# Kernel optimization log

Measured on AMD Instinct MI355X. Metric: run time of the kernel, lower is better.

The kernel has to match this reference:

```python
import jax, jax.numpy as jnp
import numpy as np

D_MODEL = 1024
N_HEADS = 16
D_K = D_MODEL // N_HEADS


def setup_inputs() -> dict:
    key = jax.random.key(0)
    k1, k2, k3, k4, k5 = jax.random.split(key, 5)
    B, S = 2, 2048
    scale = 1.0 / np.sqrt(D_MODEL)
    return {
        "query": jax.random.normal(k1, (B, S, D_MODEL), dtype=jnp.float32),
        "mask": jnp.ones((B, S, S), dtype=jnp.int32),
        "W_qkv": jax.random.normal(k2, (D_MODEL, 3 * D_MODEL), dtype=jnp.float32) * scale,
        "b_qkv": jax.random.normal(k3, (3 * D_MODEL,), dtype=jnp.float32) * 0.02,
        "W_out": jax.random.normal(k4, (D_MODEL, D_MODEL), dtype=jnp.float32) * scale,
        "b_out": jax.random.normal(k5, (D_MODEL,), dtype=jnp.float32) * 0.02,
    }


def reference(query, mask, W_qkv, b_qkv, W_out, b_out):
    B, S, _ = query.shape
    # fused QKV projection (all from query, matching the torch module)
    qkv = query @ W_qkv + b_qkv                      # [B, S, 3*D]
    q, k, v = jnp.split(qkv, 3, axis=-1)
    # [B, H, S, d_k]
    q = q.reshape(B, S, N_HEADS, D_K).transpose(0, 2, 1, 3)
    k = k.reshape(B, S, N_HEADS, D_K).transpose(0, 2, 1, 3)
    v = v.reshape(B, S, N_HEADS, D_K).transpose(0, 2, 1, 3)
    # scaled dot-product attention with explicit scores
    scores = jnp.einsum("bhqd,bhkd->bhqk", q, k) / jnp.sqrt(jnp.float32(D_K))
    m = mask[:, None, :, :]                           # [B, 1, S, S] broadcast over heads
    scores = jnp.where(m == 0, jnp.float32(-1e9), scores)
    attn = jax.nn.softmax(scores, axis=-1)           # dropout p=0 in eval -> identity
    ctx = jnp.einsum("bhqk,bhkd->bhqd", attn, v)     # [B, H, S, d_k]
    ctx = ctx.transpose(0, 2, 1, 3).reshape(B, S, D_MODEL)
    return ctx @ W_out + b_out
```

## Files before the change

kernel.cpp:

```cpp
#include <hip/hip_runtime.h>
#include <stdint.h>
#include <stddef.h>

#define S_LEN 2048
#define NB    2
#define DM    1024
#define NH    16
#define DKH   64
#define NTOK  4096
#define QKV_N 3072
#define QSCALE 0.18033688f

typedef __attribute__((ext_vector_type(4))) float floatx4;
using half2v = __attribute__((ext_vector_type(2))) _Float16;
using half4v = __attribute__((ext_vector_type(4))) _Float16;
using half8v = __attribute__((ext_vector_type(8))) _Float16;
using fp16x2 = __attribute__((ext_vector_type(2))) __fp16;

#if __has_builtin(__builtin_amdgcn_exp2f)
#define EXP2F __builtin_amdgcn_exp2f
#else
#define EXP2F exp2f
#endif

__device__ __forceinline__ void glds16(const void* g, void* l) {
    __builtin_amdgcn_global_load_lds((const __attribute__((address_space(1))) void*)g,
                                     (__attribute__((address_space(3))) void*)l,
                                     16, 0, 0);
}

__global__ __launch_bounds__(256) void cast_f16_kernel(const float* __restrict__ in,
                                                       _Float16* __restrict__ out, int n4) {
    int i = blockIdx.x * blockDim.x + threadIdx.x;
    if (i < n4) {
        float4 v = ((const float4*)in)[i];
        half4v o = {(_Float16)v.x, (_Float16)v.y, (_Float16)v.z, (_Float16)v.w};
        ((half4v*)out)[i] = o;
    }
}

__global__ __launch_bounds__(1024) void transpose_cast_kernel(const float* __restrict__ in,
                                                              _Float16* __restrict__ out,
                                                              int R, int C) {
    __shared__ float t[32][33];
    int c0 = blockIdx.x * 32, r0 = blockIdx.y * 32;
    int x = threadIdx.x, y = threadIdx.y;
    t[y][x] = in[(size_t)(r0 + y) * C + c0 + x];
    __syncthreads();
    out[(size_t)(c0 + y) * R + r0 + x] = (_Float16)t[x][y];
}

__global__ __launch_bounds__(256) void mask_reduce_kernel(const int* __restrict__ mask,
                                                          int* __restrict__ f, int n4) {
    int i = blockIdx.x * blockDim.x + threadIdx.x;
    if (i < n4) {
        int4 v = ((const int4*)mask)[i];
        if (v.x == 0 || v.y == 0 || v.z == 0 || v.w == 0) *f = 0;
    }
}

template <int FINAL, int BN>
__global__ __launch_bounds__(256) void gemm_bt_kernel(const _Float16* __restrict__ A,
                                                      const _Float16* __restrict__ Bt,
                                                      const float* __restrict__ bias,
                                                      float* __restrict__ Cf,
                                                      _Float16* __restrict__ Ch,
                                                      _Float16* __restrict__ Vt,
                                                      int M, int N, int K) {
    constexpr int NJ = BN / 32;
    __shared__ _Float16 As[128 * 64];
    __shared__ _Float16 Bs[BN * 64];

    const int nt = blockIdx.x, mt = blockIdx.y;
    const int tid = threadIdx.x, wave = tid >> 6, lane = tid & 63;
    const int quad = lane >> 4, l16 = lane & 15;
    const int wm = wave >> 1, wn = wave & 1;

    floatx4 acc[4][NJ];
    #pragma unroll
    for (int i = 0; i < 4; ++i)
        #pragma unroll
        for (int j = 0; j < NJ; ++j)
            #pragma unroll
            for (int r = 0; r < 4; ++r) acc[i][j][r] = 0.0f;

    const _Float16* Ab = A + (size_t)mt * 128 * K;
    const _Float16* Bb = Bt + (size_t)nt * BN * K;

    for (int kt = 0; kt < K; kt += 64) {
        #pragma unroll
        for (int p = 0; p < 4; ++p) {
            int slot = p * 256 + wave * 64 + lane;
            int row = slot >> 3, cc = slot & 7, c = cc ^ (row & 7);
            glds16(Ab + (size_t)row * K + kt + c * 8, As + (size_t)(p * 256 + wave * 64) * 8);
        }
        #pragma unroll
        for (int p = 0; p < BN / 32; ++p) {
            int slot = p * 256 + wave * 64 + lane;
            int row = slot >> 3, cc = slot & 7, c = cc ^ (row & 7);
            glds16(Bb + (size_t)row * K + kt + c * 8, Bs + (size_t)(p * 256 + wave * 64) * 8);
        }
        __syncthreads();

        #pragma unroll
        for (int kk = 0; kk < 2; ++kk) {
            half8v af[4], bfr[NJ];
            #pragma unroll
            for (int i = 0; i < 4; ++i) {
                int row = wm * 64 + i * 16 + l16;
                int c = (kk * 4 + quad) ^ (row & 7);
                af[i] = *(const half8v*)(As + row * 64 + c * 8);
            }
            #pragma unroll
            for (int j = 0; j < NJ; ++j) {
                int row = wn * (BN / 2) + j * 16 + l16;
                int c = (kk * 4 + quad) ^ (row & 7);
                bfr[j] = *(const half8v*)(Bs + row * 64 + c * 8);
            }
            #pragma unroll
            for (int i = 0; i < 4; ++i)
                #pragma unroll
                for (int j = 0; j < NJ; ++j)
                    acc[i][j] = __builtin_amdgcn_mfma_f32_16x16x32_f16(af[i], bfr[j], acc[i][j], 0, 0, 0);
        }
        __syncthreads();
    }

    #pragma unroll
    for (int j = 0; j < NJ; ++j) {
        int n = nt * BN + wn * (BN / 2) + j * 16 + l16;
        float bv = bias[n];
        #pragma unroll
        for (int i = 0; i < 4; ++i) {
            int m0 = mt * 128 + wm * 64 + i * 16 + quad * 4;
            float v[4];
            #pragma unroll
            for (int r = 0; r < 4; ++r) v[r] = acc[i][j][r] + bv;
            if (FINAL) {
                #pragma unroll
                for (int r = 0; r < 4; ++r) Cf[(size_t)(m0 + r) * N + n] = v[r];
            } else {
                if (n < DM) {
                    #pragma unroll
                    for (int r = 0; r < 4; ++r) v[r] *= QSCALE;
                }
                if (n < 2 * DM) {
                    #pragma unroll
                    for (int r = 0; r < 4; ++r)
                        Ch[(size_t)(m0 + r) * QKV_N + n] = (_Float16)v[r];
                } else {
                    int bb = m0 >> 11, s = m0 & (S_LEN - 1);
                    half4v t = {(_Float16)v[0], (_Float16)v[1], (_Float16)v[2], (_Float16)v[3]};
                    *(half4v*)(Vt + ((size_t)bb * (NH * DKH) + (n - 2 * DM)) * S_LEN + s) = t;
                }
            }
        }
    }
}

__global__ __launch_bounds__(128) void flash_kernel(const _Float16* __restrict__ qkv,
                                                    const _Float16* __restrict__ vt,
                                                    const int* __restrict__ mask,
                                                    const int* __restrict__ flag,
                                                    _Float16* __restrict__ ctx) {
    __shared__ _Float16 Ks[128 * 64];
    __shared__ _Float16 Vs[64 * 128];

    const int bh = blockIdx.x, qt = blockIdx.y;
    const int b = bh >> 4, h = bh & 15;
    const int tid = threadIdx.x, wave = tid >> 6, lane = tid & 63;
    const int quad = lane >> 4, l16 = lane & 15;
    const int allones = (*flag != 0);

    half8v qf0[4], qf1[4];
    #pragma unroll
    for (int G = 0; G < 4; ++G) {
        const _Float16* qr = qkv + (size_t)(b * S_LEN + qt * 128 + wave * 64 + G * 16 + l16) * QKV_N + h * DKH;
        qf0[G] = *(const half8v*)(qr + quad * 8);
        qf1[G] = *(const half8v*)(qr + 32 + quad * 8);
    }

    const _Float16* kbase = qkv + (size_t)b * S_LEN * QKV_N + DM + h * DKH;
    const _Float16* vbase = vt + (size_t)(b * NH + h) * DKH * S_LEN;

    floatx4 o[4][4];
    #pragma unroll
    for (int G = 0; G < 4; ++G)
        #pragma unroll
        for (int c = 0; c < 4; ++c)
            #pragma unroll
            for (int r = 0; r < 4; ++r) o[G][c][r] = 0.0f;
    float ls[4] = {0.0f, 0.0f, 0.0f, 0.0f};

    for (int kt = 0; kt < S_LEN / 128; ++kt) {
        #pragma unroll
        for (int p = 0; p < 8; ++p) {
            int slot = p * 128 + tid;
            int row = slot >> 3, cc = slot & 7, c = cc ^ (row & 7);
            glds16(kbase + (size_t)(kt * 128 + row) * QKV_N + c * 8, Ks + (size_t)slot * 8);
        }
        #pragma unroll
        for (int p = 0; p < 8; ++p) {
            int slot = p * 128 + tid;
            int row = slot >> 4, cc = slot & 15, c = cc ^ (row & 15);
            glds16(vbase + (size_t)row * S_LEN + kt * 128 + c * 8, Vs + (size_t)slot * 8);
        }
        __syncthreads();

        #pragma unroll
        for (int j = 0; j < 8; ++j) {
            int rowk = j * 16 + l16;
            half8v a0 = *(const half8v*)(Ks + rowk * 64 + ((quad) ^ (rowk & 7)) * 8);
            half8v a1 = *(const half8v*)(Ks + rowk * 64 + ((4 + quad) ^ (rowk & 7)) * 8);

            half4v pk[4];
            #pragma unroll
            for (int G = 0; G < 4; ++G) {
                floatx4 z;
                #pragma unroll
                for (int r = 0; r < 4; ++r) z[r] = 0.0f;
                z = __builtin_amdgcn_mfma_f32_16x16x32_f16(a0, qf0[G], z, 0, 0, 0);
                z = __builtin_amdgcn_mfma_f32_16x16x32_f16(a1, qf1[G], z, 0, 0, 0);

                if (!allones) {
                    for (int r = 0; r < 4; ++r) {
                        int s = kt * 128 + j * 16 + quad * 4 + r;
                        int qA = qt * 128 + wave * 64 + G * 16 + l16;
                        if (mask[((size_t)b * S_LEN + qA) * S_LEN + s] == 0) z[r] = -1e9f;
                    }
                }

                float p0 = EXP2F(z[0]), p1 = EXP2F(z[1]), p2 = EXP2F(z[2]), p3 = EXP2F(z[3]);
                ls[G] += (p0 + p1) + (p2 + p3);
                fp16x2 lo = __builtin_amdgcn_cvt_pkrtz(p0, p1);
                fp16x2 hi = __builtin_amdgcn_cvt_pkrtz(p2, p3);
                half2v lo2 = __builtin_bit_cast(half2v, lo);
                half2v hi2 = __builtin_bit_cast(half2v, hi);
                half4v pkg = {lo2.x, lo2.y, hi2.x, hi2.y};
                pk[G] = pkg;
            }

            int g = 2 * j + (quad >> 1);
            #pragma unroll
            for (int c = 0; c < 4; ++c) {
                int rowv = c * 16 + l16;
                half4v bv = *(const half4v*)(Vs + rowv * 128 + ((g ^ (rowv & 15)) * 8) + (quad & 1) * 4);
                #pragma unroll
                for (int G = 0; G < 4; ++G)
                    o[G][c] = __builtin_amdgcn_mfma_f32_16x16x16f16(pk[G], bv, o[G][c], 0, 0, 0);
            }
        }
        __syncthreads();
    }

    #pragma unroll
    for (int G = 0; G < 4; ++G) {
        float l = ls[G];
        l += __shfl_xor(l, 16);
        l += __shfl_xor(l, 32);
        float linv[4];
        #pragma unroll
        for (int r = 0; r < 4; ++r)
            linv[r] = 1.0f / __shfl(l, (lane & 48) | ((lane >> 4) * 4 + r));
        #pragma unroll
        for (int c = 0; c < 4; ++c)
            #pragma unroll
            for (int r = 0; r < 4; ++r) {
                int qA = qt * 128 + wave * 64 + G * 16 + quad * 4 + r;
                ctx[(size_t)(b * S_LEN + qA) * DM + h * DKH + c * 16 + l16] =
                    (_Float16)(o[G][c][r] * linv[r]);
            }
    }
}

extern "C" void kernel_launch(void* const* d_in, const int* in_sizes, int n_in,
                              void* d_out, int out_size, void* d_ws, size_t ws_size,
                              hipStream_t stream) {
    const float* query = (const float*)d_in[0];
    const int*   mask  = (const int*)d_in[1];
    const float* W_qkv = (const float*)d_in[2];
    const float* b_qkv = (const float*)d_in[3];
    const float* W_out = (const float*)d_in[4];
    const float* b_out = (const float*)d_in[5];
    float* out = (float*)d_out;

    char* w = (char*)d_ws;
    _Float16* qh   = (_Float16*)w;  w += (size_t)NTOK * DM * 2;
    _Float16* wqt  = (_Float16*)w;  w += (size_t)QKV_N * DM * 2;
    _Float16* wot  = (_Float16*)w;  w += (size_t)DM * DM * 2;
    _Float16* qkvh = (_Float16*)w;  w += (size_t)NTOK * QKV_N * 2;
    _Float16* vt   = (_Float16*)w;  w += (size_t)NB * NH * DKH * S_LEN * 2;
    int*      flag = (int*)w;
    _Float16* ctxh = qh;

    cast_f16_kernel<<<(NTOK * DM / 4 + 255) / 256, 256, 0, stream>>>(query, qh, NTOK * DM / 4);
    transpose_cast_kernel<<<dim3(QKV_N / 32, DM / 32), dim3(32, 32), 0, stream>>>(W_qkv, wqt, DM, QKV_N);
    transpose_cast_kernel<<<dim3(DM / 32, DM / 32), dim3(32, 32), 0, stream>>>(W_out, wot, DM, DM);
    hipMemsetAsync(flag, 1, 4, stream);
    mask_reduce_kernel<<<(NB * S_LEN * S_LEN / 4 + 255) / 256, 256, 0, stream>>>(
        mask, flag, NB * S_LEN * S_LEN / 4);

    gemm_bt_kernel<0, 128><<<dim3(QKV_N / 128, NTOK / 128), 256, 0, stream>>>(
        qh, wqt, b_qkv, nullptr, qkvh, vt, NTOK, QKV_N, DM);

    flash_kernel<<<dim3(NB * NH, S_LEN / 128), 128, 0, stream>>>(qkvh, vt, mask, flag, ctxh);

    gemm_bt_kernel<1, 64><<<dim3(DM / 64, NTOK / 128), 256, 0, stream>>>(
        ctxh, wot, b_out, out, nullptr, nullptr, NTOK, DM, DM);
}
```

Before: 232.1 us.

## Split attention over two key ranges with a combine kernel; separate V transpose

The flash kernel now splits the key/value sequence into two halves along a third grid dimension. Each half writes a normalized partial output and its row sum to workspace, and a new combine kernel blends the two by their sums. This doubles the number of attention blocks, so the GPU's compute units are better filled. The V transpose also moves out of the QKV GEMM epilogue into its own kernel, which simplifies that epilogue's stores. The cost is two extra launches and extra global traffic for the partial results. The blend is only exact if both halves share the same softmax reference max.

After: 252.3 us. +8.7%, slower.

```diff
diff --git a/kernel.cpp b/kernel.cpp
--- a/kernel.cpp
+++ b/kernel.cpp
@@ -59,13 +59,34 @@
     }
 }
 
+__global__ __launch_bounds__(256) void transpose_v_kernel(const _Float16* __restrict__ qkv,
+                                                          _Float16* __restrict__ vt) {
+    __shared__ _Float16 t[64][68];
+    int st = blockIdx.x * 64, h = blockIdx.y, b = blockIdx.z;
+    int tid = threadIdx.x;
+    #pragma unroll
+    for (int p = 0; p < 4; ++p) {
+        int idx = p * 1024 + tid * 4;
+        int sl = idx >> 6, d0 = idx & 63;
+        half4v v = *(const half4v*)(qkv + (size_t)(b * S_LEN + st + sl) * QKV_N + 2 * DM + h * DKH + d0);
+        t[d0 + 0][sl] = v.x; t[d0 + 1][sl] = v.y; t[d0 + 2][sl] = v.z; t[d0 + 3][sl] = v.w;
+    }
+    __syncthreads();
+    #pragma unroll
+    for (int p = 0; p < 4; ++p) {
+        int idx = p * 1024 + tid * 4;
+        int d = idx >> 6, s0 = idx & 63;
+        half4v v = {t[d][s0], t[d][s0 + 1], t[d][s0 + 2], t[d][s0 + 3]};
+        *(half4v*)(vt + ((size_t)(b * NH + h) * DKH + d) * S_LEN + st + s0) = v;
+    }
+}
+
 template <int FINAL, int BN>
 __global__ __launch_bounds__(256) void gemm_bt_kernel(const _Float16* __restrict__ A,
                                                       const _Float16* __restrict__ Bt,
                                                       const float* __restrict__ bias,
                                                       float* __restrict__ Cf,
                                                       _Float16* __restrict__ Ch,
-                                                      _Float16* __restrict__ Vt,
                                                       int M, int N, int K) {
     constexpr int NJ = BN / 32;
     __shared__ _Float16 As[128 * 64];
@@ -130,29 +151,15 @@
     for (int j = 0; j < NJ; ++j) {
         int n = nt * BN + wn * (BN / 2) + j * 16 + l16;
         float bv = bias[n];
+        float sc = (!FINAL && n < DM) ? QSCALE : 1.0f;
         #pragma unroll
         for (int i = 0; i < 4; ++i) {
             int m0 = mt * 128 + wm * 64 + i * 16 + quad * 4;
-            float v[4];
-            #pragma unroll
-            for (int r = 0; r < 4; ++r) v[r] = acc[i][j][r] + bv;
-            if (FINAL) {
-                #pragma unroll
-                for (int r = 0; r < 4; ++r) Cf[(size_t)(m0 + r) * N + n] = v[r];
-            } else {
-                if (n < DM) {
-                    #pragma unroll
-                    for (int r = 0; r < 4; ++r) v[r] *= QSCALE;
-                }
-                if (n < 2 * DM) {
-                    #pragma unroll
-                    for (int r = 0; r < 4; ++r)
-                        Ch[(size_t)(m0 + r) * QKV_N + n] = (_Float16)v[r];
-                } else {
-                    int bb = m0 >> 11, s = m0 & (S_LEN - 1);
-                    half4v t = {(_Float16)v[0], (_Float16)v[1], (_Float16)v[2], (_Float16)v[3]};
-                    *(half4v*)(Vt + ((size_t)bb * (NH * DKH) + (n - 2 * DM)) * S_LEN + s) = t;
-                }
+            #pragma unroll
+            for (int r = 0; r < 4; ++r) {
+                float v = (acc[i][j][r] + bv) * sc;
+                if (FINAL) Cf[(size_t)(m0 + r) * N + n] = v;
+                else       Ch[(size_t)(m0 + r) * QKV_N + n] = (_Float16)v;
             }
         }
     }
@@ -162,11 +169,12 @@
                                                     const _Float16* __restrict__ vt,
                                                     const int* __restrict__ mask,
                                                     const int* __restrict__ flag,
-                                                    _Float16* __restrict__ ctx) {
+                                                    _Float16* __restrict__ Opart,
+                                                    float* __restrict__ Lpart) {
     __shared__ _Float16 Ks[128 * 64];
     __shared__ _Float16 Vs[64 * 128];
 
-    const int bh = blockIdx.x, qt = blockIdx.y;
+    const int bh = blockIdx.x, qt = blockIdx.y, ks = blockIdx.z;
     const int b = bh >> 4, h = bh & 15;
     const int tid = threadIdx.x, wave = tid >> 6, lane = tid & 63;
     const int quad = lane >> 4, l16 = lane & 15;
@@ -192,7 +200,7 @@
             for (int r = 0; r < 4; ++r) o[G][c][r] = 0.0f;
     float ls[4] = {0.0f, 0.0f, 0.0f, 0.0f};
 
-    for (int kt = 0; kt < S_LEN / 128; ++kt) {
+    for (int kt = ks * 8; kt < ks * 8 + 8; ++kt) {
         #pragma unroll
         for (int p = 0; p < 8; ++p) {
             int slot = p * 128 + tid;
@@ -253,6 +261,8 @@
         __syncthreads();
     }
 
+    const size_t obase = ((size_t)(ks * 32 + bh) * 16 + qt) * (128 * 64);
+    const int lbase = ((ks * 32 + bh) * 16 + qt) * 128;
     #pragma unroll
     for (int G = 0; G < 4; ++G) {
         float l = ls[G];
@@ -260,16 +270,45 @@
         l += __shfl_xor(l, 32);
         float linv[4];
         #pragma unroll
-        for (int r = 0; r < 4; ++r)
-            linv[r] = 1.0f / __shfl(l, (lane & 48) | ((lane >> 4) * 4 + r));
+        for (int r = 0; r < 4; ++r) {
+            float lr = __shfl(l, (lane & 48) | ((lane >> 4) * 4 + r));
+            linv[r] = lr > 0.0f ? 1.0f / lr : 0.0f;
+        }
         #pragma unroll
         for (int c = 0; c < 4; ++c)
             #pragma unroll
             for (int r = 0; r < 4; ++r) {
-                int qA = qt * 128 + wave * 64 + G * 16 + quad * 4 + r;
-                ctx[(size_t)(b * S_LEN + qA) * DM + h * DKH + c * 16 + l16] =
-                    (_Float16)(o[G][c][r] * linv[r]);
-            }
+                int qq = wave * 64 + G * 16 + quad * 4 + r;
+                Opart[obase + (size_t)qq * 64 + c * 16 + l16] = (_Float16)(o[G][c][r] * linv[r]);
+            }
+        if (quad == 0) Lpart[lbase + wave * 64 + G * 16 + l16] = l;
+    }
+}
+
+__global__ __launch_bounds__(256) void combine_kernel(const _Float16* __restrict__ Opart,
+                                                      const float* __restrict__ Lpart,
+                                                      _Float16* __restrict__ ctx) {
+    const int bh = blockIdx.x, qt = blockIdx.y;
+    const int b = bh >> 4, h = bh & 15;
+    const _Float16* Oa = Opart + ((size_t)(0 * 32 + bh) * 16 + qt) * (128 * 64);
+    const _Float16* Ob = Opart + ((size_t)(1 * 32 + bh) * 16 + qt) * (128 * 64);
+    const float* La = Lpart + ((0 * 32 + bh) * 16 + qt) * 128;
+    const float* Lb = Lpart + ((1 * 32 + bh) * 16 + qt) * 128;
+    #pragma unroll
+    for (int k = 0; k < 4; ++k) {
+        int i8 = k * 256 + threadIdx.x;
+        int q = i8 >> 3, d0 = (i8 & 7) * 8;
+        float la = La[q], lb = Lb[q];
+        float s = la + lb;
+        float w = s > 0.0f ? 1.0f / s : 0.0f;
+        float wa = la * w, wb = lb * w;
+        half8v va = *(const half8v*)(Oa + (size_t)i8 * 8);
+        half8v vb = *(const half8v*)(Ob + (size_t)i8 * 8);
+        half8v o;
+        #pragma unroll
+        for (int e = 0; e < 8; ++e)
+            o[e] = (_Float16)((float)va[e] * wa + (float)vb[e] * wb);
+        *(half8v*)(ctx + (size_t)(b * S_LEN + qt * 128 + q) * DM + h * DKH + d0) = o;
     }
 }
 
@@ -285,12 +324,14 @@
     float* out = (float*)d_out;
 
     char* w = (char*)d_ws;
-    _Float16* qh   = (_Float16*)w;  w += (size_t)NTOK * DM * 2;
-    _Float16* wqt  = (_Float16*)w;  w += (size_t)QKV_N * DM * 2;
-    _Float16* wot  = (_Float16*)w;  w += (size_t)DM * DM * 2;
-    _Float16* qkvh = (_Float16*)w;  w += (size_t)NTOK * QKV_N * 2;
-    _Float16* vt   = (_Float16*)w;  w += (size_t)NB * NH * DKH * S_LEN * 2;
-    int*      flag = (int*)w;
+    _Float16* qh    = (_Float16*)w;  w += (size_t)NTOK * DM * 2;
+    _Float16* wqt   = (_Float16*)w;  w += (size_t)QKV_N * DM * 2;
+    _Float16* wot   = (_Float16*)w;  w += (size_t)DM * DM * 2;
+    _Float16* qkvh  = (_Float16*)w;  w += (size_t)NTOK * QKV_N * 2;
+    _Float16* vt    = (_Float16*)w;  w += (size_t)NB * NH * DKH * S_LEN * 2;
+    _Float16* Opart = (_Float16*)w;  w += (size_t)2 * NB * NH * 16 * 128 * 64 * 2;
+    float*    Lpart = (float*)w;     w += (size_t)2 * NB * NH * 16 * 128 * 4;
+    int*      flag  = (int*)w;
     _Float16* ctxh = qh;
 
     cast_f16_kernel<<<(NTOK * DM / 4 + 255) / 256, 256, 0, stream>>>(query, qh, NTOK * DM / 4);
@@ -301,10 +342,15 @@
         mask, flag, NB * S_LEN * S_LEN / 4);
 
     gemm_bt_kernel<0, 128><<<dim3(QKV_N / 128, NTOK / 128), 256, 0, stream>>>(
-        qh, wqt, b_qkv, nullptr, qkvh, vt, NTOK, QKV_N, DM);
-
-    flash_kernel<<<dim3(NB * NH, S_LEN / 128), 128, 0, stream>>>(qkvh, vt, mask, flag, ctxh);
+        qh, wqt, b_qkv, nullptr, qkvh, NTOK, QKV_N, DM);
+
+    transpose_v_kernel<<<dim3(S_LEN / 64, NH, NB), 256, 0, stream>>>(qkvh, vt);
+
+    flash_kernel<<<dim3(NB * NH, S_LEN / 128, 2), 128, 0, stream>>>(
+        qkvh, vt, mask, flag, Opart, Lpart);
+
+    combine_kernel<<<dim3(NB * NH, S_LEN / 128), 256, 0, stream>>>(Opart, Lpart, ctxh);
 
     gemm_bt_kernel<1, 64><<<dim3(DM / 64, NTOK / 128), 256, 0, stream>>>(
-        ctxh, wot, b_out, out, nullptr, nullptr, NTOK, DM, DM);
-}
+        ctxh, wot, b_out, out, nullptr, NTOK, DM, DM);
+}
```
